# Kernel tuning notes

Measured on AMD Instinct MI355X. Metric: run time of the kernel, lower is better.

Reference implementation:

```python
import jax, jax.numpy as jnp
import numpy as np

N, E, G = 100000, 3200000, 128
F, H = 9, 64


def _lin(key, fan_in, fan_out):
    s = 1.0 / np.sqrt(fan_in)
    k1, k2 = jax.random.split(key)
    W = jax.random.uniform(k1, (fan_in, fan_out), minval=-s, maxval=s, dtype=jnp.float32)
    b = jax.random.uniform(k2, (fan_out,), minval=-s, maxval=s, dtype=jnp.float32)
    return W, b


def setup_inputs() -> dict:
    key = jax.random.key(0)
    ks = jax.random.split(key, 16)
    x = jax.random.normal(ks[0], (N, F), dtype=jnp.float32)
    edge_index = jax.random.randint(ks[1], (2, E), 0, N, dtype=jnp.int64)
    edge_attr = jax.random.normal(ks[2], (E, 1), dtype=jnp.float32)
    batch = jnp.sort(jax.random.randint(ks[3], (N,), 0, G, dtype=jnp.int64))
    B_total = jax.random.uniform(ks[4], (G,), dtype=jnp.float32)
    terminal_mask = jax.random.randint(ks[5], (N,), 0, 2, dtype=jnp.int32)
    c_cost = jax.random.uniform(ks[6], (N,), dtype=jnp.float32)
    We1, be1 = _lin(ks[7], 1, F)   # GINEConv edge projection edge_dim->in_channels
    W1a, b1a = _lin(ks[8], F, H)
    W1b, b1b = _lin(ks[9], H, H)
    We2, be2 = _lin(ks[10], 1, H)
    W2a, b2a = _lin(ks[11], H, H)
    W2b, b2b = _lin(ks[12], H, H)
    Wr1, br1 = _lin(ks[13], H, H // 2)
    Wr2, br2 = _lin(ks[14], H // 2, 1)
    return dict(x=x, edge_index=edge_index, edge_attr=edge_attr, batch=batch,
                B_total=B_total, terminal_mask=terminal_mask, c_cost=c_cost,
                We1=We1, be1=be1, W1a=W1a, b1a=b1a, W1b=W1b, b1b=b1b,
                We2=We2, be2=be2, W2a=W2a, b2a=b2a, W2b=W2b, b2b=b2b,
                Wr1=Wr1, br1=br1, Wr2=Wr2, br2=br2)


def _gine_conv(h, src, dst, edge_attr, We, be, Wa, ba, Wb, bb):
    # GINEConv (eps=0): nn((1+eps)*x_i + sum_j ReLU(x_j + Lin(edge_attr)))
    ea = edge_attr @ We + be                      # [E, dim]
    msg = jax.nn.relu(h[src] + ea)                # gather + edge fuse + relu
    agg = jax.ops.segment_sum(msg, dst, num_segments=N)  # scatter-add
    z = h + agg
    z = jax.nn.relu(z @ Wa + ba)
    return jax.nn.relu(z @ Wb + bb)


def reference(x, edge_index, edge_attr, batch, B_total, terminal_mask, c_cost,
              We1, be1, W1a, b1a, W1b, b1b, We2, be2, W2a, b2a, W2b, b2b,
              Wr1, br1, Wr2, br2):
    src, dst = edge_index[0], edge_index[1]
    h = _gine_conv(x, src, dst, edge_attr, We1, be1, W1a, b1a, W1b, b1b)
    h = _gine_conv(h, src, dst, edge_attr, We2, be2, W2a, b2a, W2b, b2b)
    pi_raw = jax.nn.sigmoid(jax.nn.relu(h @ Wr1 + br1) @ Wr2 + br2)[:, 0]  # [N]
    pi_raw = pi_raw * (1.0 - terminal_mask.astype(pi_raw.dtype))
    node_expenses = pi_raw * c_cost
    total_expenses = jax.ops.segment_sum(node_expenses, batch, num_segments=B_total.shape[0])
    ratio = jnp.minimum(B_total[batch] / (total_expenses[batch] + 1e-12), 1.0)
    return pi_raw * ratio
```

## Files before the change

kernel.cpp:

```cpp
#include <hip/hip_runtime.h>
#include <hip/hip_fp16.h>
#include <math.h>

#define TPB 256
#define P_BLOCKS 512
#define BSHIFT 8
#define BINS_MAX 512

struct alignas(8)  h2x2 { __half2 a, b; };
struct alignas(16) h2x4 { __half2 a, b, c, d; };

typedef _Float16 f16;
typedef __attribute__((ext_vector_type(8))) _Float16 f16x8;
typedef __attribute__((ext_vector_type(4))) float f32x4;

#define MFMA16(a, b, c) __builtin_amdgcn_mfma_f32_16x16x32_f16(a, b, c, 0, 0, 0)

__global__ void __launch_bounds__(256) k_bhist(const int* __restrict__ dst,
                                               int* __restrict__ counts, int E, int B) {
  __shared__ int h[BINS_MAX];
  int t = threadIdx.x, blk = blockIdx.x;
  for (int i = t; i < B; i += TPB) h[i] = 0;
  __syncthreads();
  int chunk = (E + P_BLOCKS - 1) / P_BLOCKS;
  int s = blk * chunk, e = min(E, s + chunk);
  for (int i = s + t; i < e; i += TPB)
    atomicAdd(&h[__builtin_nontemporal_load(&dst[i]) >> BSHIFT], 1);
  __syncthreads();
  for (int i = t; i < B; i += TPB) counts[i * P_BLOCKS + blk] = h[i];
}

__global__ void k_scan_block(const int* __restrict__ deg, int* __restrict__ offs,
                             int* __restrict__ bsums, int n) {
  __shared__ int lds[256];
  int t = threadIdx.x, b = blockIdx.x;
  int base = b * 1024 + t * 4;
  int v0 = (base + 0 < n) ? deg[base + 0] : 0;
  int v1 = (base + 1 < n) ? deg[base + 1] : 0;
  int v2 = (base + 2 < n) ? deg[base + 2] : 0;
  int v3 = (base + 3 < n) ? deg[base + 3] : 0;
  int s = v0 + v1 + v2 + v3;
  lds[t] = s;
  __syncthreads();
  int acc = s;
  for (int off = 1; off < 256; off <<= 1) {
    int x = (t >= off) ? lds[t - off] : 0;
    __syncthreads();
    acc += x;
    lds[t] = acc;
    __syncthreads();
  }
  int excl = acc - s;
  if (base + 0 < n) offs[base + 0] = excl;
  if (base + 1 < n) offs[base + 1] = excl + v0;
  if (base + 2 < n) offs[base + 2] = excl + v0 + v1;
  if (base + 3 < n) offs[base + 3] = excl + v0 + v1 + v2;
  if (t == 255) bsums[b] = acc;
}

__global__ void k_scan_mid(int* __restrict__ bsums, int nb) {
  __shared__ int lds[256];
  int t = threadIdx.x;
  int v = (t < nb) ? bsums[t] : 0;
  lds[t] = v;
  __syncthreads();
  int acc = v;
  for (int off = 1; off < 256; off <<= 1) {
    int x = (t >= off) ? lds[t - off] : 0;
    __syncthreads();
    acc += x;
    lds[t] = acc;
    __syncthreads();
  }
  if (t < nb) bsums[t] = acc - v;
}

__global__ void k_scan_add(int* __restrict__ offs, const int* __restrict__ bsums,
                           int n, int total) {
  int t = threadIdx.x, b = blockIdx.x;
  int add = bsums[b];
  int base = b * 1024 + t * 4;
#pragma unroll
  for (int j = 0; j < 4; ++j)
    if (base + j < n) offs[base + j] += add;
  if (b == 0 && t == 0) offs[n] = total;
}

__global__ void __launch_bounds__(256) k_bfill(const int* __restrict__ src,
                                               const int* __restrict__ dst,
                                               const float* __restrict__ attr,
                                               const int* __restrict__ offs,
                                               int2* __restrict__ ebuf, int E, int B) {
  __shared__ int cur[BINS_MAX];
  int t = threadIdx.x, blk = blockIdx.x;
  for (int i = t; i < B; i += TPB) cur[i] = offs[i * P_BLOCKS + blk];
  __syncthreads();
  int chunk = (E + P_BLOCKS - 1) / P_BLOCKS;
  int s = blk * chunk, e = min(E, s + chunk);
#pragma unroll 4
  for (int i = s + t; i < e; i += TPB) {
    int d = __builtin_nontemporal_load(&dst[i]);
    int sv = __builtin_nontemporal_load(&src[i]);
    float av = __builtin_nontemporal_load(&attr[i]);
    int bin = d >> BSHIFT;
    int pos = atomicAdd(&cur[bin], 1);
    ebuf[pos] = make_int2((sv << BSHIFT) | (d & ((1 << BSHIFT) - 1)), __float_as_int(av));
  }
}

__global__ void __launch_bounds__(256) k_bsort(const long long* __restrict__ ebuf,
                                               const int* __restrict__ offs,
                                               int2* __restrict__ csr,
                                               int* __restrict__ noffs,
                                               int N, int E) {
  __shared__ int hist[256];
  __shared__ int cursor[256];
  __shared__ int sc[256];
  int t = threadIdx.x, bkt = blockIdx.x;
  hist[t] = 0;
  __syncthreads();
  int s = offs[bkt * P_BLOCKS], e = offs[(bkt + 1) * P_BLOCKS];
#pragma unroll 4
  for (int i = s + t; i < e; i += TPB) {
    long long pv = __builtin_nontemporal_load(&ebuf[i]);
    int key = (int)(unsigned int)(pv & 0xffffffffLL);
    atomicAdd(&hist[key & 255], 1);
  }
  __syncthreads();
  int v = hist[t];
  int acc = v;
  sc[t] = v;
  __syncthreads();
  for (int off = 1; off < 256; off <<= 1) {
    int x = (t >= off) ? sc[t - off] : 0;
    __syncthreads();
    acc += x;
    sc[t] = acc;
    __syncthreads();
  }
  int base = s + acc - v;
  cursor[t] = base;
  int n = (bkt << BSHIFT) + t;
  if (n < N) noffs[n] = base;
  if (bkt == 0 && t == 0) noffs[N] = E;
  __syncthreads();
#pragma unroll 4
  for (int i = s + t; i < e; i += TPB) {
    long long pv = __builtin_nontemporal_load(&ebuf[i]);
    int key = (int)(unsigned int)(pv & 0xffffffffLL);
    int attr = (int)(unsigned int)(((unsigned long long)pv) >> 32);
    int pos = atomicAdd(&cursor[key & 255], 1);
    csr[pos] = make_int2(((unsigned int)key) >> BSHIFT, attr);
  }
}

__global__ void __launch_bounds__(256) k_agg1(
    const float* __restrict__ x, const int2* __restrict__ csr,
    const int* __restrict__ noffs, const float* __restrict__ We1,
    const float* __restrict__ be1, float* __restrict__ u1, int N) {
  int t = blockIdx.x * TPB + threadIdx.x;
  int node = t >> 4, f = t & 15;
  if (node >= N || f >= 9) return;
  int o0 = noffs[node], o1 = noffs[node + 1];
  float we = We1[f], be = be1[f];
  float acc = 0.f;
  int e = o0;
  for (; e + 3 < o1; e += 4) {
    int2 p0 = csr[e], p1 = csr[e + 1], p2 = csr[e + 2], p3 = csr[e + 3];
    float v0 = x[p0.x * 9 + f] + fmaf(__int_as_float(p0.y), we, be);
    float v1 = x[p1.x * 9 + f] + fmaf(__int_as_float(p1.y), we, be);
    float v2 = x[p2.x * 9 + f] + fmaf(__int_as_float(p2.y), we, be);
    float v3 = x[p3.x * 9 + f] + fmaf(__int_as_float(p3.y), we, be);
    acc += fmaxf(v0, 0.f) + fmaxf(v1, 0.f) + fmaxf(v2, 0.f) + fmaxf(v3, 0.f);
  }
  for (; e < o1; ++e) {
    int2 p = csr[e];
    acc += fmaxf(x[p.x * 9 + f] + fmaf(__int_as_float(p.y), we, be), 0.f);
  }
  u1[node * 9 + f] = x[node * 9 + f] + acc;
}

__global__ void __launch_bounds__(256) k_agg2(
    const __half* __restrict__ h1, const long long* __restrict__ csr,
    const int* __restrict__ noffs, const float* __restrict__ We2,
    const float* __restrict__ be2, float* __restrict__ u2, int N) {
  int gt = blockIdx.x * TPB + threadIdx.x;
  int node = gt >> 6;
  if (node >= N) return;
  int lane = gt & 63;
  int q = lane >> 3, c = lane & 7;
  float4 weA = *(const float4*)&We2[c * 8];
  float4 weB = *(const float4*)&We2[c * 8 + 4];
  float4 beA = *(const float4*)&be2[c * 8];
  float4 beB = *(const float4*)&be2[c * 8 + 4];
  int o0 = noffs[node], o1 = noffs[node + 1];
  float a0 = 0.f, a1 = 0.f, a2 = 0.f, a3 = 0.f, a4 = 0.f, a5 = 0.f, a6 = 0.f, a7 = 0.f;

#define AGG2_ACCM(pv, v, m)                                                  \
  {                                                                          \
    float ea = __int_as_float((int)(unsigned int)(((unsigned long long)(pv)) >> 32)); \
    float2 f0 = __half22float2((v).a), f1 = __half22float2((v).b);           \
    float2 f2 = __half22float2((v).c), f3 = __half22float2((v).d);           \
    a0 += (m) ? fmaxf(f0.x + fmaf(ea, weA.x, beA.x), 0.f) : 0.f;             \
    a1 += (m) ? fmaxf(f0.y + fmaf(ea, weA.y, beA.y), 0.f) : 0.f;             \
    a2 += (m) ? fmaxf(f1.x + fmaf(ea, weA.z, beA.z), 0.f) : 0.f;             \
    a3 += (m) ? fmaxf(f1.y + fmaf(ea, weA.w, beA.w), 0.f) : 0.f;             \
    a4 += (m) ? fmaxf(f2.x + fmaf(ea, weB.x, beB.x), 0.f) : 0.f;             \
    a5 += (m) ? fmaxf(f2.y + fmaf(ea, weB.y, beB.y), 0.f) : 0.f;             \
    a6 += (m) ? fmaxf(f3.x + fmaf(ea, weB.z, beB.z), 0.f) : 0.f;             \
    a7 += (m) ? fmaxf(f3.y + fmaf(ea, weB.w, beB.w), 0.f) : 0.f;             \
  }

  int e = o0;
  if (o1 - e > 32) {
    int last = o1 - 1;
    do {
      long long pv0, pv1, pv2, pv3, pv4, pv5, pv6, pv7;
      bool m0, m1, m2, m3, m4, m5, m6, m7;
      {
        int i0 = e + q;      m0 = i0 < o1; i0 = m0 ? i0 : last;
        int i1 = e + 8 + q;  m1 = i1 < o1; i1 = m1 ? i1 : last;
        int i2 = e + 16 + q; m2 = i2 < o1; i2 = m2 ? i2 : last;
        int i3 = e + 24 + q; m3 = i3 < o1; i3 = m3 ? i3 : last;
        int i4 = e + 32 + q; m4 = i4 < o1; i4 = m4 ? i4 : last;
        int i5 = e + 40 + q; m5 = i5 < o1; i5 = m5 ? i5 : last;
        int i6 = e + 48 + q; m6 = i6 < o1; i6 = m6 ? i6 : last;
        int i7 = e + 56 + q; m7 = i7 < o1; i7 = m7 ? i7 : last;
        pv0 = __builtin_nontemporal_load(&csr[i0]);
        pv1 = __builtin_nontemporal_load(&csr[i1]);
        pv2 = __builtin_nontemporal_load(&csr[i2]);
        pv3 = __builtin_nontemporal_load(&csr[i3]);
        pv4 = __builtin_nontemporal_load(&csr[i4]);
        pv5 = __builtin_nontemporal_load(&csr[i5]);
        pv6 = __builtin_nontemporal_load(&csr[i6]);
        pv7 = __builtin_nontemporal_load(&csr[i7]);
      }
      h2x4 v0 = *(const h2x4*)(h1 + (size_t)(int)(unsigned int)(pv0 & 0xffffffffLL) * 64 + c * 8);
      h2x4 v1 = *(const h2x4*)(h1 + (size_t)(int)(unsigned int)(pv1 & 0xffffffffLL) * 64 + c * 8);
      h2x4 v2 = *(const h2x4*)(h1 + (size_t)(int)(unsigned int)(pv2 & 0xffffffffLL) * 64 + c * 8);
      h2x4 v3 = *(const h2x4*)(h1 + (size_t)(int)(unsigned int)(pv3 & 0xffffffffLL) * 64 + c * 8);
      h2x4 v4 = *(const h2x4*)(h1 + (size_t)(int)(unsigned int)(pv4 & 0xffffffffLL) * 64 + c * 8);
      h2x4 v5 = *(const h2x4*)(h1 + (size_t)(int)(unsigned int)(pv5 & 0xffffffffLL) * 64 + c * 8);
      h2x4 v6 = *(const h2x4*)(h1 + (size_t)(int)(unsigned int)(pv6 & 0xffffffffLL) * 64 + c * 8);
      h2x4 v7 = *(const h2x4*)(h1 + (size_t)(int)(unsigned int)(pv7 & 0xffffffffLL) * 64 + c * 8);
      AGG2_ACCM(pv0, v0, m0); AGG2_ACCM(pv1, v1, m1);
      AGG2_ACCM(pv2, v2, m2); AGG2_ACCM(pv3, v3, m3);
      AGG2_ACCM(pv4, v4, m4); AGG2_ACCM(pv5, v5, m5);
      AGG2_ACCM(pv6, v6, m6); AGG2_ACCM(pv7, v7, m7);
      e += 64;
    } while (o1 - e > 32);
  }
  if (e < o1) {
    int last = o1 - 1;
    int i0 = e + q;      bool m0 = i0 < o1; i0 = m0 ? i0 : last;
    int i1 = e + 8 + q;  bool m1 = i1 < o1; i1 = m1 ? i1 : last;
    int i2 = e + 16 + q; bool m2 = i2 < o1; i2 = m2 ? i2 : last;
    int i3 = e + 24 + q; bool m3 = i3 < o1; i3 = m3 ? i3 : last;
    long long pv0 = __builtin_nontemporal_load(&csr[i0]);
    long long pv1 = __builtin_nontemporal_load(&csr[i1]);
    long long pv2 = __builtin_nontemporal_load(&csr[i2]);
    long long pv3 = __builtin_nontemporal_load(&csr[i3]);
    h2x4 v0 = *(const h2x4*)(h1 + (size_t)(int)(unsigned int)(pv0 & 0xffffffffLL) * 64 + c * 8);
    h2x4 v1 = *(const h2x4*)(h1 + (size_t)(int)(unsigned int)(pv1 & 0xffffffffLL) * 64 + c * 8);
    h2x4 v2 = *(const h2x4*)(h1 + (size_t)(int)(unsigned int)(pv2 & 0xffffffffLL) * 64 + c * 8);
    h2x4 v3 = *(const h2x4*)(h1 + (size_t)(int)(unsigned int)(pv3 & 0xffffffffLL) * 64 + c * 8);
    AGG2_ACCM(pv0, v0, m0); AGG2_ACCM(pv1, v1, m1);
    AGG2_ACCM(pv2, v2, m2); AGG2_ACCM(pv3, v3, m3);
  }
#undef AGG2_ACCM

  a0 += __shfl_xor(a0, 8, 64); a0 += __shfl_xor(a0, 16, 64); a0 += __shfl_xor(a0, 32, 64);
  a1 += __shfl_xor(a1, 8, 64); a1 += __shfl_xor(a1, 16, 64); a1 += __shfl_xor(a1, 32, 64);
  a2 += __shfl_xor(a2, 8, 64); a2 += __shfl_xor(a2, 16, 64); a2 += __shfl_xor(a2, 32, 64);
  a3 += __shfl_xor(a3, 8, 64); a3 += __shfl_xor(a3, 16, 64); a3 += __shfl_xor(a3, 32, 64);
  a4 += __shfl_xor(a4, 8, 64); a4 += __shfl_xor(a4, 16, 64); a4 += __shfl_xor(a4, 32, 64);
  a5 += __shfl_xor(a5, 8, 64); a5 += __shfl_xor(a5, 16, 64); a5 += __shfl_xor(a5, 32, 64);
  a6 += __shfl_xor(a6, 8, 64); a6 += __shfl_xor(a6, 16, 64); a6 += __shfl_xor(a6, 32, 64);
  a7 += __shfl_xor(a7, 8, 64); a7 += __shfl_xor(a7, 16, 64); a7 += __shfl_xor(a7, 32, 64);

  if (q == 0) {
    h2x4 sf = *(const h2x4*)(h1 + (size_t)node * 64 + c * 8);
    float2 s0 = __half22float2(sf.a), s1 = __half22float2(sf.b);
    float2 s2 = __half22float2(sf.c), s3 = __half22float2(sf.d);
    float4 oA, oB;
    oA.x = s0.x + a0; oA.y = s0.y + a1; oA.z = s1.x + a2; oA.w = s1.y + a3;
    oB.x = s2.x + a4; oB.y = s2.y + a5; oB.z = s3.x + a6; oB.w = s3.y + a7;
    *(float4*)&u2[(size_t)node * 64 + c * 8] = oA;
    *(float4*)&u2[(size_t)node * 64 + c * 8 + 4] = oB;
  }
}

__device__ __forceinline__ void splitf8(const float* v, f16x8& h, f16x8& l) {
#pragma unroll
  for (int j = 0; j < 8; ++j) {
    float x = v[j];
    f16 hh = (f16)x;
    h[j] = hh;
    l[j] = (f16)(x - (float)hh);
  }
}

__device__ __forceinline__ void pack_w(const float* __restrict__ W, int Ntiles, int nslots,
                                       f16* hi, f16* lo, int t) {
  int lane = t & 63;
  int kg = lane >> 4, m = lane & 15;
  int Nout = Ntiles * 16;
  for (int s = t >> 6; s < nslots; s += 4) {
    int ks = s / Ntiles, nt = s - ks * Ntiles;
    int kbase = ks * 32 + kg * 8;
    int n = nt * 16 + m;
    float v[8];
#pragma unroll
    for (int j = 0; j < 8; ++j) v[j] = W[(kbase + j) * Nout + n];
    f16x8 h, l;
    splitf8(v, h, l);
    *(f16x8*)&hi[(s * 64 + lane) * 8] = h;
    *(f16x8*)&lo[(s * 64 + lane) * 8] = l;
  }
}

__global__ void __launch_bounds__(256) k_mlp9(
    const float* __restrict__ uin, const float* __restrict__ Wa,
    const float* __restrict__ ba, const float* __restrict__ Wb,
    const float* __restrict__ bb, __half* __restrict__ hout, int N) {
  __shared__ __align__(16) f16 wf1h[2048], wf1l[2048];
  __shared__ __align__(16) f16 wf2h[4096], wf2l[4096];
  __shared__ float ls_z[64 * 65];
  __shared__ float ls_ba[64], ls_bb[64];
  const int t = threadIdx.x;
  const int n0 = blockIdx.x * 64;
  const int w = t >> 6, lane = t & 63;
  const int m = lane & 15, kg = lane >> 4;

  {
    int s = w;
    int n = s * 16 + m;
    float v[8];
#pragma unroll
    for (int j = 0; j < 8; ++j) {
      int k = kg * 8 + j;
      v[j] = (k < 9) ? Wa[k * 64 + n] : 0.f;
    }
    f16x8 h, l;
    splitf8(v, h, l);
    *(f16x8*)&wf1h[(s * 64 + lane) * 8] = h;
    *(f16x8*)&wf1l[(s * 64 + lane) * 8] = l;
  }
  pack_w(Wb, 4, 8, wf2h, wf2l, t);
  if (t < 64) { ls_ba[t] = ba[t]; ls_bb[t] = bb[t]; }
  __syncthreads();

  int row = min(n0 + w * 16 + m, N - 1);
  float av[8];
#pragma unroll
  for (int j = 0; j < 8; ++j) {
    int k = kg * 8 + j;
    av[j] = (k < 9) ? uin[(size_t)row * 9 + k] : 0.f;
  }
  f16x8 a0h, a0l, a1h, a1l;
  splitf8(av, a0h, a0l);

  f32x4 acc[4];
#pragma unroll
  for (int nt = 0; nt < 4; ++nt) { f32x4 z4 = {0.f, 0.f, 0.f, 0.f}; acc[nt] = z4; }
#pragma unroll
  for (int nt = 0; nt < 4; ++nt) {
    f16x8 bh = *(const f16x8*)&wf1h[(nt * 64 + lane) * 8];
    f16x8 bl = *(const f16x8*)&wf1l[(nt * 64 + lane) * 8];
    acc[nt] = MFMA16(a0h, bh, acc[nt]);
    acc[nt] = MFMA16(a0l, bh, acc[nt]);
    acc[nt] = MFMA16(a0h, bl, acc[nt]);
  }
#pragma unroll
  for (int nt = 0; nt < 4; ++nt)
#pragma unroll
    for (int r = 0; r < 4; ++r)
      ls_z[(w * 16 + kg * 4 + r) * 65 + nt * 16 + m] = fmaxf(acc[nt][r] + ls_ba[nt * 16 + m], 0.f);
  __syncthreads();

  const float* zr = &ls_z[(size_t)(w * 16 + m) * 65 + kg * 8];
  {
    float zv0[8], zv1[8];
#pragma unroll
    for (int j = 0; j < 8; ++j) { zv0[j] = zr[j]; zv1[j] = zr[32 + j]; }
    splitf8(zv0, a0h, a0l);
    splitf8(zv1, a1h, a1l);
  }
#pragma unroll
  for (int nt = 0; nt < 4; ++nt) { f32x4 z4 = {0.f, 0.f, 0.f, 0.f}; acc[nt] = z4; }
#pragma unroll
  for (int nt = 0; nt < 4; ++nt) {
#pragma unroll
    for (int ks = 0; ks < 2; ++ks) {
      int s = ks * 4 + nt;
      f16x8 bh = *(const f16x8*)&wf2h[(s * 64 + lane) * 8];
      f16x8 bl = *(const f16x8*)&wf2l[(s * 64 + lane) * 8];
      f16x8 ah = ks ? a1h : a0h;
      f16x8 al = ks ? a1l : a0l;
      acc[nt] = MFMA16(ah, bh, acc[nt]);
      acc[nt] = MFMA16(al, bh, acc[nt]);
      acc[nt] = MFMA16(ah, bl, acc[nt]);
    }
  }
#pragma unroll
  for (int nt = 0; nt < 4; ++nt)
#pragma unroll
    for (int r = 0; r < 4; ++r) {
      int node = n0 + w * 16 + kg * 4 + r;
      if (node < N)
        hout[(size_t)node * 64 + nt * 16 + m] =
            __float2half(fmaxf(acc[nt][r] + ls_bb[nt * 16 + m], 0.f));
    }
}

__global__ void __launch_bounds__(256) k_mlp_ro(
    const float* __restrict__ uin, const float* __restrict__ Wa,
    const float* __restrict__ ba, const float* __restrict__ Wb,
    const float* __restrict__ bb, const float* __restrict__ Wr1,
    const float* __restrict__ br1, const float* __restrict__ Wr2,
    const float* __restrict__ br2, const int* __restrict__ tmask,
    float* __restrict__ pi, int N) {
  __shared__ __align__(16) f16 wf1h[4096], wf1l[4096];
  __shared__ __align__(16) f16 wf2h[4096], wf2l[4096];
  __shared__ __align__(16) f16 wfrh[2048], wfrl[2048];
  __shared__ float ls_z[64 * 65];
  __shared__ float ls_ba[64], ls_bb[64], ls_br1[32], ls_w2[32];
  const int t = threadIdx.x;
  const int n0 = blockIdx.x * 64;

  pack_w(Wa, 4, 8, wf1h, wf1l, t);
  pack_w(Wb, 4, 8, wf2h, wf2l, t);
  pack_w(Wr1, 2, 4, wfrh, wfrl, t);
  if (t < 64) { ls_ba[t] = ba[t]; ls_bb[t] = bb[t]; }
  else if (t < 96) { ls_br1[t - 64] = br1[t - 64]; ls_w2[t - 64] = Wr2[t - 64]; }
  __syncthreads();

  const int w = t >> 6, lane = t & 63;
  const int m = lane & 15, kg = lane >> 4;

  int row = n0 + w * 16 + m;
  row = min(row, N - 1);
  const float* ar = uin + (size_t)row * 64 + kg * 8;
  float av0[8], av1[8];
  {
    f32x4 p0 = *(const f32x4*)ar;
    f32x4 p1 = *(const f32x4*)(ar + 4);
    f32x4 p2 = *(const f32x4*)(ar + 32);
    f32x4 p3 = *(const f32x4*)(ar + 36);
#pragma unroll
    for (int j = 0; j < 4; ++j) {
      av0[j] = p0[j]; av0[4 + j] = p1[j];
      av1[j] = p2[j]; av1[4 + j] = p3[j];
    }
  }
  f16x8 a0h, a0l, a1h, a1l;
  splitf8(av0, a0h, a0l);
  splitf8(av1, a1h, a1l);

  f32x4 acc[4];
#pragma unroll
  for (int nt = 0; nt < 4; ++nt) { f32x4 z4 = {0.f, 0.f, 0.f, 0.f}; acc[nt] = z4; }
#pragma unroll
  for (int nt = 0; nt < 4; ++nt) {
#pragma unroll
    for (int ks = 0; ks < 2; ++ks) {
      int s = ks * 4 + nt;
      f16x8 bh = *(const f16x8*)&wf1h[(s * 64 + lane) * 8];
      f16x8 bl = *(const f16x8*)&wf1l[(s * 64 + lane) * 8];
      f16x8 ah = ks ? a1h : a0h;
      f16x8 al = ks ? a1l : a0l;
      acc[nt] = MFMA16(ah, bh, acc[nt]);
      acc[nt] = MFMA16(al, bh, acc[nt]);
      acc[nt] = MFMA16(ah, bl, acc[nt]);
    }
  }
#pragma unroll
  for (int nt = 0; nt < 4; ++nt)
#pragma unroll
    for (int r = 0; r < 4; ++r)
      ls_z[(w * 16 + kg * 4 + r) * 65 + nt * 16 + m] = fmaxf(acc[nt][r] + ls_ba[nt * 16 + m], 0.f);
  __syncthreads();

  const float* zr = &ls_z[(size_t)(w * 16 + m) * 65 + kg * 8];
  {
    float zv0[8], zv1[8];
#pragma unroll
    for (int j = 0; j < 8; ++j) { zv0[j] = zr[j]; zv1[j] = zr[32 + j]; }
    splitf8(zv0, a0h, a0l);
    splitf8(zv1, a1h, a1l);
  }
#pragma unroll
  for (int nt = 0; nt < 4; ++nt) { f32x4 z4 = {0.f, 0.f, 0.f, 0.f}; acc[nt] = z4; }
#pragma unroll
  for (int nt = 0; nt < 4; ++nt) {
#pragma unroll
    for (int ks = 0; ks < 2; ++ks) {
      int s = ks * 4 + nt;
      f16x8 bh = *(const f16x8*)&wf2h[(s * 64 + lane) * 8];
      f16x8 bl = *(const f16x8*)&wf2l[(s * 64 + lane) * 8];
      f16x8 ah = ks ? a1h : a0h;
      f16x8 al = ks ? a1l : a0l;
      acc[nt] = MFMA16(ah, bh, acc[nt]);
      acc[nt] = MFMA16(al, bh, acc[nt]);
      acc[nt] = MFMA16(ah, bl, acc[nt]);
    }
  }
  __syncthreads();
#pragma unroll
  for (int nt = 0; nt < 4; ++nt)
#pragma unroll
    for (int r = 0; r < 4; ++r)
      ls_z[(w * 16 + kg * 4 + r) * 65 + nt * 16 + m] = fmaxf(acc[nt][r] + ls_bb[nt * 16 + m], 0.f);
  __syncthreads();

  {
    float zv0[8], zv1[8];
#pragma unroll
    for (int j = 0; j < 8; ++j) { zv0[j] = zr[j]; zv1[j] = zr[32 + j]; }
    splitf8(zv0, a0h, a0l);
    splitf8(zv1, a1h, a1l);
  }
  f32x4 accr[2];
#pragma unroll
  for (int nt = 0; nt < 2; ++nt) { f32x4 z4 = {0.f, 0.f, 0.f, 0.f}; accr[nt] = z4; }
#pragma unroll
  for (int nt = 0; nt < 2; ++nt) {
#pragma unroll
    for (int ks = 0; ks < 2; ++ks) {
      int s = ks * 2 + nt;
      f16x8 bh = *(const f16x8*)&wfrh[(s * 64 + lane) * 8];
      f16x8 bl = *(const f16x8*)&wfrl[(s * 64 + lane) * 8];
      f16x8 ah = ks ? a1h : a0h;
      f16x8 al = ks ? a1l : a0l;
      accr[nt] = MFMA16(ah, bh, accr[nt]);
      accr[nt] = MFMA16(al, bh, accr[nt]);
      accr[nt] = MFMA16(ah, bl, accr[nt]);
    }
  }
  float b2 = br2[0];
#pragma unroll
  for (int r = 0; r < 4; ++r) {
    float v0 = fmaxf(accr[0][r] + ls_br1[m], 0.f) * ls_w2[m];
    float v1 = fmaxf(accr[1][r] + ls_br1[16 + m], 0.f) * ls_w2[16 + m];
    float tr = v0 + v1;
    tr += __shfl_xor(tr, 1, 64);
    tr += __shfl_xor(tr, 2, 64);
    tr += __shfl_xor(tr, 4, 64);
    tr += __shfl_xor(tr, 8, 64);
    if (m == 0) {
      int node = n0 + w * 16 + kg * 4 + r;
      if (node < N) {
        float sg = 1.f / (1.f + expf(-(tr + b2)));
        pi[node] = sg * (1.f - (float)tmask[node]);
      }
    }
  }
}

__global__ void k_grpsum(const float* __restrict__ pi, const float* __restrict__ c_cost,
                         const int* __restrict__ batch, float* __restrict__ exp_tot, int N) {
  __shared__ float lsf[256];
  __shared__ int lsi[256];
  int t = threadIdx.x;
  int i = blockIdx.x * TPB + t;
  bool valid = i < N;
  int g = valid ? batch[i] : 0;
  float v = valid ? pi[i] * c_cost[i] : 0.f;
  lsi[t] = valid ? g : 0x7fffffff;
  __syncthreads();
  for (int s = 128; s > 0; s >>= 1) { if (t < s) lsi[t] = min(lsi[t], lsi[t + s]); __syncthreads(); }
  int gmin = lsi[0];
  __syncthreads();
  lsi[t] = valid ? g : -1;
  __syncthreads();
  for (int s = 128; s > 0; s >>= 1) { if (t < s) lsi[t] = max(lsi[t], lsi[t + s]); __syncthreads(); }
  int gmax = lsi[0];
  __syncthreads();
  for (int gg = gmin; gg <= gmax; ++gg) {
    lsf[t] = (valid && g == gg) ? v : 0.f;
    __syncthreads();
    for (int s = 128; s > 0; s >>= 1) { if (t < s) lsf[t] += lsf[t + s]; __syncthreads(); }
    if (t == 0) atomicAdd(&exp_tot[gg], lsf[0]);
    __syncthreads();
  }
}

__global__ void k_final(const float* __restrict__ pi, const int* __restrict__ batch,
                        const float* __restrict__ B_total, const float* __restrict__ exp_tot,
                        float* __restrict__ out, int N) {
  int i = blockIdx.x * TPB + threadIdx.x;
  if (i < N) {
    int g = batch[i];
    float ratio = fminf(B_total[g] / (exp_tot[g] + 1e-12f), 1.f);
    out[i] = pi[i] * ratio;
  }
}

extern "C" void kernel_launch(void* const* d_in, const int* in_sizes, int n_in,
                              void* d_out, int out_size, void* d_ws, size_t ws_size,
                              hipStream_t stream) {
  const float* x     = (const float*)d_in[0];
  const int*   ei    = (const int*)d_in[1];
  const float* eattr = (const float*)d_in[2];
  const int*   batch = (const int*)d_in[3];
  const float* Btot  = (const float*)d_in[4];
  const int*   tmask = (const int*)d_in[5];
  const float* ccost = (const float*)d_in[6];
  const float* We1 = (const float*)d_in[7],  *be1 = (const float*)d_in[8];
  const float* W1a = (const float*)d_in[9],  *b1a = (const float*)d_in[10];
  const float* W1b = (const float*)d_in[11], *b1b = (const float*)d_in[12];
  const float* We2 = (const float*)d_in[13], *be2 = (const float*)d_in[14];
  const float* W2a = (const float*)d_in[15], *b2a = (const float*)d_in[16];
  const float* W2b = (const float*)d_in[17], *b2b = (const float*)d_in[18];
  const float* Wr1 = (const float*)d_in[19], *br1 = (const float*)d_in[20];
  const float* Wr2 = (const float*)d_in[21], *br2 = (const float*)d_in[22];
  float* out = (float*)d_out;

  const int N = in_sizes[0] / 9;
  const int E = in_sizes[2];
  const int G = in_sizes[4];
  const int* src = ei;
  const int* dst = ei + E;
  const int B = (N + (1 << BSHIFT) - 1) >> BSHIFT;
  const int nscan = B * P_BLOCKS;

  size_t cur = 0;
  auto alloc = [&](size_t elems) { size_t r = cur; cur += elems; cur = (cur + 63) & ~(size_t)63; return r; };
  char* wsb = (char*)d_ws;
  size_t o_exp    = alloc(G);
  size_t o_counts = alloc(nscan);
  size_t o_offs   = alloc(nscan + 1);
  size_t o_bsums  = alloc(256);
  size_t o_noffs  = alloc(N + 1);
  size_t o_csr    = alloc(2 * (size_t)E);
  size_t e_or_h   = (2 * (size_t)E > (size_t)N * 32) ? 2 * (size_t)E : (size_t)N * 32;
  size_t o_ebuf   = alloc(e_or_h);
  size_t o_u1     = alloc((size_t)N * 9);
  size_t o_u2     = alloc((size_t)N * 64);
  size_t o_pi     = alloc(N);
  (void)ws_size;

  float* exp_t  = (float*)wsb + o_exp;
  int*   counts = (int*)wsb + o_counts;
  int*   offs   = (int*)wsb + o_offs;
  int*   bsums  = (int*)wsb + o_bsums;
  int*   noffs  = (int*)wsb + o_noffs;
  int2*  csr    = (int2*)((int*)wsb + o_csr);
  int2*  ebuf   = (int2*)((int*)wsb + o_ebuf);
  __half* h1h   = (__half*)((int*)wsb + o_ebuf);
  float* u1     = (float*)wsb + o_u1;
  float* u2     = (float*)wsb + o_u2;
  float* pi     = (float*)wsb + o_pi;

  (void)hipMemsetAsync(exp_t, 0, (size_t)G * 4, stream);

  const int nb = (nscan + 1023) / 1024;

  k_bhist<<<P_BLOCKS, TPB, 0, stream>>>(dst, counts, E, B);
  k_scan_block<<<nb, TPB, 0, stream>>>(counts, offs, bsums, nscan);
  k_scan_mid<<<1, 256, 0, stream>>>(bsums, nb);
  k_scan_add<<<nb, TPB, 0, stream>>>(offs, bsums, nscan, E);
  k_bfill<<<P_BLOCKS, TPB, 0, stream>>>(src, dst, eattr, offs, ebuf, E, B);
  k_bsort<<<B, TPB, 0, stream>>>((const long long*)ebuf, offs, csr, noffs, N, E);

  k_agg1<<<((size_t)N * 16 + TPB - 1) / TPB, TPB, 0, stream>>>(x, csr, noffs, We1, be1, u1, N);
  k_mlp9<<<(N + 63) / 64, TPB, 0, stream>>>(u1, W1a, b1a, W1b, b1b, h1h, N);

  k_agg2<<<((size_t)N * 64 + TPB - 1) / TPB, TPB, 0, stream>>>(h1h, (const long long*)csr, noffs, We2, be2, u2, N);
  k_mlp_ro<<<(N + 63) / 64, TPB, 0, stream>>>(u2, W2a, b2a, W2b, b2b, Wr1, br1, Wr2, br2, tmask, pi, N);

  k_grpsum<<<(N + TPB - 1) / TPB, TPB, 0, stream>>>(pi, ccost, batch, exp_t, N);
  k_final<<<(N + TPB - 1) / TPB, TPB, 0, stream>>>(pi, batch, Btot, exp_t, out, N);
}
```

Before: 407.4 us.

## Pad per-node CSR segments to multiples of 32 to remove masked tails

After: 454.4 us. +11.5%, slower.

```diff
diff --git a/kernel.cpp b/kernel.cpp
--- a/kernel.cpp
+++ b/kernel.cpp
@@ -6,6 +6,7 @@
 #define P_BLOCKS 512
 #define BSHIFT 8
 #define BINS_MAX 512
+#define PAD_ATTR 0x7fc00000
 
 struct alignas(8)  h2x2 { __half2 a, b; };
 struct alignas(16) h2x4 { __half2 a, b, c, d; };
@@ -58,6 +59,34 @@
   if (t == 255) bsums[b] = acc;
 }
 
+__global__ void k_scan_block_pad(const int* __restrict__ deg, int* __restrict__ offs,
+                                 int* __restrict__ bsums, int n) {
+  __shared__ int lds[256];
+  int t = threadIdx.x, b = blockIdx.x;
+  int base = b * 1024 + t * 4;
+  int v0 = (base + 0 < n) ? ((deg[base + 0] + 31) & ~31) : 0;
+  int v1 = (base + 1 < n) ? ((deg[base + 1] + 31) & ~31) : 0;
+  int v2 = (base + 2 < n) ? ((deg[base + 2] + 31) & ~31) : 0;
+  int v3 = (base + 3 < n) ? ((deg[base + 3] + 31) & ~31) : 0;
+  int s = v0 + v1 + v2 + v3;
+  lds[t] = s;
+  __syncthreads();
+  int acc = s;
+  for (int off = 1; off < 256; off <<= 1) {
+    int x = (t >= off) ? lds[t - off] : 0;
+    __syncthreads();
+    acc += x;
+    lds[t] = acc;
+    __syncthreads();
+  }
+  int excl = acc - s;
+  if (base + 0 < n) offs[base + 0] = excl;
+  if (base + 1 < n) offs[base + 1] = excl + v0;
+  if (base + 2 < n) offs[base + 2] = excl + v0 + v1;
+  if (base + 3 < n) offs[base + 3] = excl + v0 + v1 + v2;
+  if (t == 255) bsums[b] = acc;
+}
+
 __global__ void k_scan_mid(int* __restrict__ bsums, int nb) {
   __shared__ int lds[256];
   int t = threadIdx.x;
@@ -108,14 +137,10 @@
   }
 }
 
-__global__ void __launch_bounds__(256) k_bsort(const long long* __restrict__ ebuf,
-                                               const int* __restrict__ offs,
-                                               int2* __restrict__ csr,
-                                               int* __restrict__ noffs,
-                                               int N, int E) {
+__global__ void __launch_bounds__(256) k_bsort_a(const long long* __restrict__ ebuf,
+                                                 const int* __restrict__ offs,
+                                                 int* __restrict__ pdeg, int N) {
   __shared__ int hist[256];
-  __shared__ int cursor[256];
-  __shared__ int sc[256];
   int t = threadIdx.x, bkt = blockIdx.x;
   hist[t] = 0;
   __syncthreads();
@@ -123,27 +148,23 @@
 #pragma unroll 4
   for (int i = s + t; i < e; i += TPB) {
     long long pv = __builtin_nontemporal_load(&ebuf[i]);
-    int key = (int)(unsigned int)(pv & 0xffffffffLL);
-    atomicAdd(&hist[key & 255], 1);
-  }
-  __syncthreads();
-  int v = hist[t];
-  int acc = v;
-  sc[t] = v;
-  __syncthreads();
-  for (int off = 1; off < 256; off <<= 1) {
-    int x = (t >= off) ? sc[t - off] : 0;
-    __syncthreads();
-    acc += x;
-    sc[t] = acc;
-    __syncthreads();
-  }
-  int base = s + acc - v;
-  cursor[t] = base;
+    atomicAdd(&hist[(int)(pv & 255)], 1);
+  }
+  __syncthreads();
   int n = (bkt << BSHIFT) + t;
-  if (n < N) noffs[n] = base;
-  if (bkt == 0 && t == 0) noffs[N] = E;
-  __syncthreads();
+  if (n < N) pdeg[n] = hist[t];
+}
+
+__global__ void __launch_bounds__(256) k_bsort_b(const long long* __restrict__ ebuf,
+                                                 const int* __restrict__ offs,
+                                                 const int* __restrict__ noffs,
+                                                 int2* __restrict__ csr, int N) {
+  __shared__ int cursor[256];
+  int t = threadIdx.x, bkt = blockIdx.x;
+  int n = (bkt << BSHIFT) + t;
+  cursor[t] = (n < N) ? noffs[n] : 0;
+  __syncthreads();
+  int s = offs[bkt * P_BLOCKS], e = offs[(bkt + 1) * P_BLOCKS];
 #pragma unroll 4
   for (int i = s + t; i < e; i += TPB) {
     long long pv = __builtin_nontemporal_load(&ebuf[i]);
@@ -151,6 +172,11 @@
     int attr = (int)(unsigned int)(((unsigned long long)pv) >> 32);
     int pos = atomicAdd(&cursor[key & 255], 1);
     csr[pos] = make_int2(((unsigned int)key) >> BSHIFT, attr);
+  }
+  __syncthreads();
+  if (n < N) {
+    int end = noffs[n + 1];
+    for (int i = cursor[t]; i < end; ++i) csr[i] = make_int2(0, PAD_ATTR);
   }
 }
 
@@ -164,18 +190,25 @@
   int o0 = noffs[node], o1 = noffs[node + 1];
   float we = We1[f], be = be1[f];
   float acc = 0.f;
-  int e = o0;
-  for (; e + 3 < o1; e += 4) {
-    int2 p0 = csr[e], p1 = csr[e + 1], p2 = csr[e + 2], p3 = csr[e + 3];
+  for (int e = o0; e < o1; e += 8) {
+    int2 p0 = csr[e],     p1 = csr[e + 1], p2 = csr[e + 2], p3 = csr[e + 3];
+    int2 p4 = csr[e + 4], p5 = csr[e + 5], p6 = csr[e + 6], p7 = csr[e + 7];
     float v0 = x[p0.x * 9 + f] + fmaf(__int_as_float(p0.y), we, be);
     float v1 = x[p1.x * 9 + f] + fmaf(__int_as_float(p1.y), we, be);
     float v2 = x[p2.x * 9 + f] + fmaf(__int_as_float(p2.y), we, be);
     float v3 = x[p3.x * 9 + f] + fmaf(__int_as_float(p3.y), we, be);
-    acc += fmaxf(v0, 0.f) + fmaxf(v1, 0.f) + fmaxf(v2, 0.f) + fmaxf(v3, 0.f);
-  }
-  for (; e < o1; ++e) {
-    int2 p = csr[e];
-    acc += fmaxf(x[p.x * 9 + f] + fmaf(__int_as_float(p.y), we, be), 0.f);
+    float v4 = x[p4.x * 9 + f] + fmaf(__int_as_float(p4.y), we, be);
+    float v5 = x[p5.x * 9 + f] + fmaf(__int_as_float(p5.y), we, be);
+    float v6 = x[p6.x * 9 + f] + fmaf(__int_as_float(p6.y), we, be);
+    float v7 = x[p7.x * 9 + f] + fmaf(__int_as_float(p7.y), we, be);
+    acc += fmaxf(v0, 0.f);
+    acc += fmaxf(v1, 0.f);
+    acc += fmaxf(v2, 0.f);
+    acc += fmaxf(v3, 0.f);
+    acc += fmaxf(v4, 0.f);
+    acc += fmaxf(v5, 0.f);
+    acc += fmaxf(v6, 0.f);
+    acc += fmaxf(v7, 0.f);
   }
   u1[node * 9 + f] = x[node * 9 + f] + acc;
 }
@@ -196,45 +229,32 @@
   int o0 = noffs[node], o1 = noffs[node + 1];
   float a0 = 0.f, a1 = 0.f, a2 = 0.f, a3 = 0.f, a4 = 0.f, a5 = 0.f, a6 = 0.f, a7 = 0.f;
 
-#define AGG2_ACCM(pv, v, m)                                                  \
+#define AGG2_ACC(pv, v)                                                      \
   {                                                                          \
     float ea = __int_as_float((int)(unsigned int)(((unsigned long long)(pv)) >> 32)); \
     float2 f0 = __half22float2((v).a), f1 = __half22float2((v).b);           \
     float2 f2 = __half22float2((v).c), f3 = __half22float2((v).d);           \
-    a0 += (m) ? fmaxf(f0.x + fmaf(ea, weA.x, beA.x), 0.f) : 0.f;             \
-    a1 += (m) ? fmaxf(f0.y + fmaf(ea, weA.y, beA.y), 0.f) : 0.f;             \
-    a2 += (m) ? fmaxf(f1.x + fmaf(ea, weA.z, beA.z), 0.f) : 0.f;             \
-    a3 += (m) ? fmaxf(f1.y + fmaf(ea, weA.w, beA.w), 0.f) : 0.f;             \
-    a4 += (m) ? fmaxf(f2.x + fmaf(ea, weB.x, beB.x), 0.f) : 0.f;             \
-    a5 += (m) ? fmaxf(f2.y + fmaf(ea, weB.y, beB.y), 0.f) : 0.f;             \
-    a6 += (m) ? fmaxf(f3.x + fmaf(ea, weB.z, beB.z), 0.f) : 0.f;             \
-    a7 += (m) ? fmaxf(f3.y + fmaf(ea, weB.w, beB.w), 0.f) : 0.f;             \
+    a0 += fmaxf(f0.x + fmaf(ea, weA.x, beA.x), 0.f);                         \
+    a1 += fmaxf(f0.y + fmaf(ea, weA.y, beA.y), 0.f);                         \
+    a2 += fmaxf(f1.x + fmaf(ea, weA.z, beA.z), 0.f);                         \
+    a3 += fmaxf(f1.y + fmaf(ea, weA.w, beA.w), 0.f);                         \
+    a4 += fmaxf(f2.x + fmaf(ea, weB.x, beB.x), 0.f);                         \
+    a5 += fmaxf(f2.y + fmaf(ea, weB.y, beB.y), 0.f);                         \
+    a6 += fmaxf(f3.x + fmaf(ea, weB.z, beB.z), 0.f);                         \
+    a7 += fmaxf(f3.y + fmaf(ea, weB.w, beB.w), 0.f);                         \
   }
 
   int e = o0;
   if (o1 - e > 32) {
-    int last = o1 - 1;
     do {
-      long long pv0, pv1, pv2, pv3, pv4, pv5, pv6, pv7;
-      bool m0, m1, m2, m3, m4, m5, m6, m7;
-      {
-        int i0 = e + q;      m0 = i0 < o1; i0 = m0 ? i0 : last;
-        int i1 = e + 8 + q;  m1 = i1 < o1; i1 = m1 ? i1 : last;
-        int i2 = e + 16 + q; m2 = i2 < o1; i2 = m2 ? i2 : last;
-        int i3 = e + 24 + q; m3 = i3 < o1; i3 = m3 ? i3 : last;
-        int i4 = e + 32 + q; m4 = i4 < o1; i4 = m4 ? i4 : last;
-        int i5 = e + 40 + q; m5 = i5 < o1; i5 = m5 ? i5 : last;
-        int i6 = e + 48 + q; m6 = i6 < o1; i6 = m6 ? i6 : last;
-        int i7 = e + 56 + q; m7 = i7 < o1; i7 = m7 ? i7 : last;
-        pv0 = __builtin_nontemporal_load(&csr[i0]);
-        pv1 = __builtin_nontemporal_load(&csr[i1]);
-        pv2 = __builtin_nontemporal_load(&csr[i2]);
-        pv3 = __builtin_nontemporal_load(&csr[i3]);
-        pv4 = __builtin_nontemporal_load(&csr[i4]);
-        pv5 = __builtin_nontemporal_load(&csr[i5]);
-        pv6 = __builtin_nontemporal_load(&csr[i6]);
-        pv7 = __builtin_nontemporal_load(&csr[i7]);
-      }
+      long long pv0 = __builtin_nontemporal_load(&csr[e + q]);
+      long long pv1 = __builtin_nontemporal_load(&csr[e + 8 + q]);
+      long long pv2 = __builtin_nontemporal_load(&csr[e + 16 + q]);
+      long long pv3 = __builtin_nontemporal_load(&csr[e + 24 + q]);
+      long long pv4 = __builtin_nontemporal_load(&csr[e + 32 + q]);
+      long long pv5 = __builtin_nontemporal_load(&csr[e + 40 + q]);
+      long long pv6 = __builtin_nontemporal_load(&csr[e + 48 + q]);
+      long long pv7 = __builtin_nontemporal_load(&csr[e + 56 + q]);
       h2x4 v0 = *(const h2x4*)(h1 + (size_t)(int)(unsigned int)(pv0 & 0xffffffffLL) * 64 + c * 8);
       h2x4 v1 = *(const h2x4*)(h1 + (size_t)(int)(unsigned int)(pv1 & 0xffffffffLL) * 64 + c * 8);
       h2x4 v2 = *(const h2x4*)(h1 + (size_t)(int)(unsigned int)(pv2 & 0xffffffffLL) * 64 + c * 8);
@@ -243,31 +263,26 @@
       h2x4 v5 = *(const h2x4*)(h1 + (size_t)(int)(unsigned int)(pv5 & 0xffffffffLL) * 64 + c * 8);
       h2x4 v6 = *(const h2x4*)(h1 + (size_t)(int)(unsigned int)(pv6 & 0xffffffffLL) * 64 + c * 8);
       h2x4 v7 = *(const h2x4*)(h1 + (size_t)(int)(unsigned int)(pv7 & 0xffffffffLL) * 64 + c * 8);
-      AGG2_ACCM(pv0, v0, m0); AGG2_ACCM(pv1, v1, m1);
-      AGG2_ACCM(pv2, v2, m2); AGG2_ACCM(pv3, v3, m3);
-      AGG2_ACCM(pv4, v4, m4); AGG2_ACCM(pv5, v5, m5);
-      AGG2_ACCM(pv6, v6, m6); AGG2_ACCM(pv7, v7, m7);
+      AGG2_ACC(pv0, v0); AGG2_ACC(pv1, v1);
+      AGG2_ACC(pv2, v2); AGG2_ACC(pv3, v3);
+      AGG2_ACC(pv4, v4); AGG2_ACC(pv5, v5);
+      AGG2_ACC(pv6, v6); AGG2_ACC(pv7, v7);
       e += 64;
     } while (o1 - e > 32);
   }
   if (e < o1) {
-    int last = o1 - 1;
-    int i0 = e + q;      bool m0 = i0 < o1; i0 = m0 ? i0 : last;
-    int i1 = e + 8 + q;  bool m1 = i1 < o1; i1 = m1 ? i1 : last;
-    int i2 = e + 16 + q; bool m2 = i2 < o1; i2 = m2 ? i2 : last;
-    int i3 = e + 24 + q; bool m3 = i3 < o1; i3 = m3 ? i3 : last;
-    long long pv0 = __builtin_nontemporal_load(&csr[i0]);
-    long long pv1 = __builtin_nontemporal_load(&csr[i1]);
-    long long pv2 = __builtin_nontemporal_load(&csr[i2]);
-    long long pv3 = __builtin_nontemporal_load(&csr[i3]);
+    long long pv0 = __builtin_nontemporal_load(&csr[e + q]);
+    long long pv1 = __builtin_nontemporal_load(&csr[e + 8 + q]);
+    long long pv2 = __builtin_nontemporal_load(&csr[e + 16 + q]);
+    long long pv3 = __builtin_nontemporal_load(&csr[e + 24 + q]);
     h2x4 v0 = *(const h2x4*)(h1 + (size_t)(int)(unsigned int)(pv0 & 0xffffffffLL) * 64 + c * 8);
     h2x4 v1 = *(const h2x4*)(h1 + (size_t)(int)(unsigned int)(pv1 & 0xffffffffLL) * 64 + c * 8);
     h2x4 v2 = *(const h2x4*)(h1 + (size_t)(int)(unsigned int)(pv2 & 0xffffffffLL) * 64 + c * 8);
     h2x4 v3 = *(const h2x4*)(h1 + (size_t)(int)(unsigned int)(pv3 & 0xffffffffLL) * 64 + c * 8);
-    AGG2_ACCM(pv0, v0, m0); AGG2_ACCM(pv1, v1, m1);
-    AGG2_ACCM(pv2, v2, m2); AGG2_ACCM(pv3, v3, m3);
-  }
-#undef AGG2_ACCM
+    AGG2_ACC(pv0, v0); AGG2_ACC(pv1, v1);
+    AGG2_ACC(pv2, v2); AGG2_ACC(pv3, v3);
+  }
+#undef AGG2_ACC
 
   a0 += __shfl_xor(a0, 8, 64); a0 += __shfl_xor(a0, 16, 64); a0 += __shfl_xor(a0, 32, 64);
   a1 += __shfl_xor(a1, 8, 64); a1 += __shfl_xor(a1, 16, 64); a1 += __shfl_xor(a1, 32, 64);
@@ -631,37 +646,46 @@
   size_t o_counts = alloc(nscan);
   size_t o_offs   = alloc(nscan + 1);
   size_t o_bsums  = alloc(256);
-  size_t o_noffs  = alloc(N + 1);
-  size_t o_csr    = alloc(2 * (size_t)E);
-  size_t e_or_h   = (2 * (size_t)E > (size_t)N * 32) ? 2 * (size_t)E : (size_t)N * 32;
+  size_t o_pdeg   = alloc(N + 1);
+  size_t o_noffs  = alloc(N + 2);
+  size_t csr_cap  = (size_t)E + 31 * (size_t)N + 64;
+  size_t o_csr    = alloc(2 * csr_cap);
+  size_t need_hup = (size_t)N * 32 + (size_t)N * 9 + (size_t)N + 64;
+  size_t e_or_h   = (2 * (size_t)E > need_hup) ? 2 * (size_t)E : need_hup;
   size_t o_ebuf   = alloc(e_or_h);
-  size_t o_u1     = alloc((size_t)N * 9);
   size_t o_u2     = alloc((size_t)N * 64);
-  size_t o_pi     = alloc(N);
   (void)ws_size;
 
   float* exp_t  = (float*)wsb + o_exp;
   int*   counts = (int*)wsb + o_counts;
   int*   offs   = (int*)wsb + o_offs;
   int*   bsums  = (int*)wsb + o_bsums;
+  int*   pdeg   = (int*)wsb + o_pdeg;
   int*   noffs  = (int*)wsb + o_noffs;
   int2*  csr    = (int2*)((int*)wsb + o_csr);
   int2*  ebuf   = (int2*)((int*)wsb + o_ebuf);
   __half* h1h   = (__half*)((int*)wsb + o_ebuf);
-  float* u1     = (float*)wsb + o_u1;
+  float* u1     = (float*)((int*)wsb + o_ebuf + (size_t)N * 32);
+  float* pi     = (float*)((int*)wsb + o_ebuf + (size_t)N * 41);
   float* u2     = (float*)wsb + o_u2;
-  float* pi     = (float*)wsb + o_pi;
 
   (void)hipMemsetAsync(exp_t, 0, (size_t)G * 4, stream);
-
-  const int nb = (nscan + 1023) / 1024;
+  (void)hipMemsetAsync(pdeg, 0, ((size_t)N + 1) * 4, stream);
+
+  const int nb1 = (nscan + 1023) / 1024;
+  const int nb2 = (N + 1 + 1023) / 1024;
 
   k_bhist<<<P_BLOCKS, TPB, 0, stream>>>(dst, counts, E, B);
-  k_scan_block<<<nb, TPB, 0, stream>>>(counts, offs, bsums, nscan);
-  k_scan_mid<<<1, 256, 0, stream>>>(bsums, nb);
-  k_scan_add<<<nb, TPB, 0, stream>>>(offs, bsums, nscan, E);
+  k_scan_block<<<nb1, TPB, 0, stream>>>(counts, offs, bsums, nscan);
+  k_scan_mid<<<1, 256, 0, stream>>>(bsums, nb1);
+  k_scan_add<<<nb1, TPB, 0, stream>>>(offs, bsums, nscan, E);
   k_bfill<<<P_BLOCKS, TPB, 0, stream>>>(src, dst, eattr, offs, ebuf, E, B);
-  k_bsort<<<B, TPB, 0, stream>>>((const long long*)ebuf, offs, csr, noffs, N, E);
+
+  k_bsort_a<<<B, TPB, 0, stream>>>((const long long*)ebuf, offs, pdeg, N);
+  k_scan_block_pad<<<nb2, TPB, 0, stream>>>(pdeg, noffs, bsums, N + 1);
+  k_scan_mid<<<1, 256, 0, stream>>>(bsums, nb2);
+  k_scan_add<<<nb2, TPB, 0, stream>>>(noffs, bsums, N + 1, 0);
+  k_bsort_b<<<B, TPB, 0, stream>>>((const long long*)ebuf, offs, noffs, csr, N);
 
   k_agg1<<<((size_t)N * 16 + TPB - 1) / TPB, TPB, 0, stream>>>(x, csr, noffs, We1, be1, u1, N);
   k_mlp9<<<(N + 63) / 64, TPB, 0, stream>>>(u1, W1a, b1a, W1b, b1b, h1h, N);
```
